# Kernel tuning notes

Hardware: AMD Instinct MI355X
Metric: run time of the kernel (lower is better)

Reference implementation:

```python
import jax, jax.numpy as jnp
import numpy as np

NEG_INF = float('-inf')

def setup_inputs() -> dict:
    key = jax.random.key(0)
    k1, k2 = jax.random.split(key)
    B, T, S, H, D = 2, 2048, 2048, 8, 64
    q = jax.random.normal(k1, (B, T, H, D), dtype=jnp.float32)
    kv = jax.random.normal(k2, (B, S, 2, H, D), dtype=jnp.float32)
    key_padding_mask = jnp.ones((B, S), dtype=bool)  # True = valid key
    return {"q": q, "kv": kv, "key_padding_mask": key_padding_mask, "causal": 1}


def reference(q, kv, key_padding_mask, causal):
    # q: (B,T,H,D), kv: (B,S,2,H,D)
    k = kv[:, :, 0]  # (B,S,H,D)
    v = kv[:, :, 1]  # (B,S,H,D)
    D = q.shape[-1]
    scale = D ** (-0.5)
    # scores: (B,H,T,S)
    scores = jnp.einsum('bthd,bshd->bhts', q, k) * scale
    # mask: True means "mask out" (matches torch masked_fill semantics)
    mask = ~key_padding_mask[:, None, None, :]  # (B,1,1,S)
    if causal:
        T, S = scores.shape[2], scores.shape[3]
        causal_mask = jnp.triu(jnp.ones((T, S), dtype=bool), k=1)  # (T,S)
        mask = mask | causal_mask[None, None, :, :]
    scores = jnp.where(mask, NEG_INF, scores)
    attn = jax.nn.softmax(scores, axis=-1)
    out = jnp.einsum('bhts,bshd->bthd', attn, v)  # (B,T,H,D)
    return out
```

## Files before the change

### kernel.cpp

```cpp
#include <hip/hip_runtime.h>
#include <hip/hip_bf16.h>
#include <math.h>

typedef __bf16 bf8_t __attribute__((ext_vector_type(8)));
typedef float  f4_t  __attribute__((ext_vector_type(4)));

constexpr int Bc = 2;
constexpr int Tc = 2048;
constexpr int Sc = 2048;
constexpr int Hc = 8;
constexpr int Dc = 64;
constexpr int BQ = 64;
constexpr int BK = 64;
constexpr int nQB = Tc / BQ;
constexpr int LDK = Dc + 8;
constexpr int LDV = BK + 2;
constexpr int SMAX = 8;
constexpr int GPH  = 144;

union BF8U { bf8_t v; unsigned int u[4]; };

__device__ inline unsigned int pkbf(float a, float b) {
    union { __bf16 h; unsigned short s; } x, y;
    x.h = (__bf16)a; y.h = (__bf16)b;
    return (unsigned int)x.s | ((unsigned int)y.s << 16);
}

__global__ __launch_bounds__(256, 4)
void fa_part(const float* __restrict__ q,
             const float* __restrict__ kv,
             const int* __restrict__ kpm,
             const int* __restrict__ causal_p,
             float* __restrict__ part_o,
             float* __restrict__ part_l)
{
    __shared__ __bf16 Ks[BK][LDK];
    __shared__ __bf16 Vt[Dc][LDV];

    const int tid  = threadIdx.x;
    const int wave = tid >> 6;
    const int lane = tid & 63;
    const int n16  = lane & 15;
    const int quad = lane >> 4;

    const int bid = blockIdx.x;
    const int h   = bid & 7;
    const int g   = bid >> 3;
    const int b   = g / GPH;
    const int idx = g - b * GPH;
    int a = (int)((sqrtf(1.0f + 2.0f * (float)idx) - 1.0f) * 0.5f);
    while (2 * (a + 1) * (a + 2) <= idx) ++a;
    while (2 * a * (a + 1) > idx) --a;
    const int rem = idx - 2 * a * (a + 1);
    const int S   = a + 1;
    const int r0  = rem / S;
    const int s   = rem - r0 * S;
    const int qt  = 4 * a + r0;
    const int q_base = qt * BQ;
    const int causal = causal_p[0];
    const int t_row  = q_base + wave * 16 + n16;

    {
        const int row = tid >> 2, dc = (tid & 3) * 16;
        const float* qr = q + ((size_t)(b * Tc + q_base + row) * Hc + h) * Dc + dc;
        float4 x[4];
        x[0] = *(const float4*)(qr + 0);
        x[1] = *(const float4*)(qr + 4);
        x[2] = *(const float4*)(qr + 8);
        x[3] = *(const float4*)(qr + 12);
        const float* xf = (const float*)x;
        const float sc = 0.125f;
        BF8U t0v, t1v;
        #pragma unroll
        for (int i = 0; i < 4; ++i) {
            t0v.u[i] = pkbf(xf[2 * i] * sc, xf[2 * i + 1] * sc);
            t1v.u[i] = pkbf(xf[8 + 2 * i] * sc, xf[9 + 2 * i] * sc);
        }
        *(bf8_t*)&Ks[row][dc]     = t0v.v;
        *(bf8_t*)&Ks[row][dc + 8] = t1v.v;
    }
    __syncthreads();
    bf8_t b_q[2];
    b_q[0] = *(const bf8_t*)&Ks[wave * 16 + n16][quad * 8];
    b_q[1] = *(const bf8_t*)&Ks[wave * 16 + n16][32 + quad * 8];

    f4_t o_acc[4];
    #pragma unroll
    for (int dt = 0; dt < 4; ++dt) o_acc[dt] = (f4_t){0.f, 0.f, 0.f, 0.f};
    float l_p = 0.f;

    const int kend = causal ? (q_base + BQ) : Sc;
    const int ntot = kend / BK;
    const int t0   = ntot * s / S;
    const int t1   = ntot * (s + 1) / S;

    const int krow = tid >> 2, kdc = (tid & 3) * 16;
    const int vkp  = tid >> 3, vdb = (tid & 7) * 8;
    const int KSTR = 2 * Hc * Dc;
    const float* kbase = kv + ((size_t)b * Sc * 2 * Hc + h) * Dc;
    const float* vbase = kbase + (size_t)Hc * Dc;

    float4 pk4[4], pv4[4];
    {
        const int kbG = t0 * BK;
        const float* kr = kbase + (size_t)(kbG + krow) * KSTR + kdc;
        pk4[0] = *(const float4*)(kr + 0);  pk4[1] = *(const float4*)(kr + 4);
        pk4[2] = *(const float4*)(kr + 8);  pk4[3] = *(const float4*)(kr + 12);
        const float* v0 = vbase + (size_t)(kbG + 2 * vkp) * KSTR + vdb;
        const float* v1 = v0 + KSTR;
        pv4[0] = *(const float4*)(v0 + 0);  pv4[1] = *(const float4*)(v0 + 4);
        pv4[2] = *(const float4*)(v1 + 0);  pv4[3] = *(const float4*)(v1 + 4);
    }

    for (int it = t0; it < t1; ++it) {
        const int kbG = it * BK;

        __syncthreads();

        {
            const float* kf = (const float*)pk4;
            BF8U w0, w1;
            #pragma unroll
            for (int i = 0; i < 4; ++i) {
                w0.u[i] = pkbf(kf[2 * i], kf[2 * i + 1]);
                w1.u[i] = pkbf(kf[8 + 2 * i], kf[9 + 2 * i]);
            }
            *(bf8_t*)&Ks[krow][kdc]     = w0.v;
            *(bf8_t*)&Ks[krow][kdc + 8] = w1.v;
            const float* vvf = (const float*)pv4;
            #pragma unroll
            for (int j = 0; j < 8; ++j) {
                *(unsigned int*)&Vt[vdb + j][2 * vkp] = pkbf(vvf[j], vvf[8 + j]);
            }
        }
        __syncthreads();

        if (it + 1 < t1) {
            const int nkb = kbG + BK;
            const float* kr = kbase + (size_t)(nkb + krow) * KSTR + kdc;
            pk4[0] = *(const float4*)(kr + 0);  pk4[1] = *(const float4*)(kr + 4);
            pk4[2] = *(const float4*)(kr + 8);  pk4[3] = *(const float4*)(kr + 12);
            const float* v0 = vbase + (size_t)(nkb + 2 * vkp) * KSTR + vdb;
            const float* v1 = v0 + KSTR;
            pv4[0] = *(const float4*)(v0 + 0);  pv4[1] = *(const float4*)(v0 + 4);
            pv4[2] = *(const float4*)(v1 + 0);  pv4[3] = *(const float4*)(v1 + 4);
        }

        f4_t sacc[4];
        #pragma unroll
        for (int u = 0; u < 4; ++u) {
            const bf8_t ak0 = *(const bf8_t*)&Ks[16 * u + n16][quad * 8];
            const bf8_t ak1 = *(const bf8_t*)&Ks[16 * u + n16][32 + quad * 8];
            f4_t acc = (f4_t){0.f, 0.f, 0.f, 0.f};
            acc = __builtin_amdgcn_mfma_f32_16x16x32_bf16(ak0, b_q[0], acc, 0, 0, 0);
            acc = __builtin_amdgcn_mfma_f32_16x16x32_bf16(ak1, b_q[1], acc, 0, 0, 0);
            sacc[u] = acc;
        }

        unsigned int pp[4][2];
        #pragma unroll
        for (int u = 0; u < 4; ++u) {
            const int4 mw = *(const int4*)&kpm[b * Sc + kbG + 16 * u + 4 * quad];
            float p[4];
            #pragma unroll
            for (int r = 0; r < 4; ++r) {
                const int key = kbG + 16 * u + 4 * quad + r;
                const bool valid = ((&mw.x)[r] != 0) && (!causal || key <= t_row);
                p[r] = valid ? __expf(sacc[u][r] - 8.0f) : 0.0f;
                l_p += p[r];
            }
            pp[u][0] = pkbf(p[0], p[1]);
            pp[u][1] = pkbf(p[2], p[3]);
        }

        const int sl0 = (2 * (quad & 1)) * 16 + n16;
        const int sl1 = sl0 + 16;
        int y[4][4];
        #pragma unroll
        for (int u = 0; u < 4; ++u) {
            y[u][0] = __shfl((int)pp[u][0], sl0, 64);
            y[u][1] = __shfl((int)pp[u][1], sl0, 64);
            y[u][2] = __shfl((int)pp[u][0], sl1, 64);
            y[u][3] = __shfl((int)pp[u][1], sl1, 64);
        }
        const bool hi = quad >= 2;
        BF8U bp0, bp1;
        #pragma unroll
        for (int i = 0; i < 4; ++i) {
            bp0.u[i] = (unsigned)(hi ? y[1][i] : y[0][i]);
            bp1.u[i] = (unsigned)(hi ? y[3][i] : y[2][i]);
        }

        #pragma unroll
        for (int dt = 0; dt < 4; ++dt) {
            const bf8_t av0 = *(const bf8_t*)&Vt[dt * 16 + n16][quad * 8];
            const bf8_t av1 = *(const bf8_t*)&Vt[dt * 16 + n16][32 + quad * 8];
            o_acc[dt] = __builtin_amdgcn_mfma_f32_16x16x32_bf16(av0, bp0.v, o_acc[dt], 0, 0, 0);
            o_acc[dt] = __builtin_amdgcn_mfma_f32_16x16x32_bf16(av1, bp1.v, o_acc[dt], 0, 0, 0);
        }
    }

    float l1 = l_p + __shfl_xor(l_p, 16, 64);
    const float l_tot = l1 + __shfl_xor(l1, 32, 64);

    const int qi  = (b * Hc + h) * nQB + qt;
    const int row = wave * 16 + n16;
    float* po = part_o + ((size_t)qi * SMAX + s) * (BQ * Dc);
    #pragma unroll
    for (int dt = 0; dt < 4; ++dt) {
        *(f4_t*)(po + row * Dc + dt * 16 + 4 * quad) = o_acc[dt];
    }
    if (quad == 0) {
        part_l[((size_t)qi * SMAX + s) * BQ + row] = l_tot;
    }
}

__global__ __launch_bounds__(256, 4)
void fa_reduce(const float* __restrict__ part_o,
               const float* __restrict__ part_l,
               float* __restrict__ out)
{
    const int gtid = blockIdx.x * 256 + threadIdx.x;
    const int e    = gtid & (BQ * Dc / 4 - 1);
    const int qi   = gtid >> 10;
    const int row  = e >> 4;
    const int d4   = e & 15;
    const int qt   = qi & (nQB - 1);
    const int S    = (qt >> 2) + 1;

    float4 acc = make_float4(0.f, 0.f, 0.f, 0.f);
    float  l   = 0.f;
    for (int s = 0; s < S; ++s) {
        const size_t pi = (size_t)qi * SMAX + s;
        const float4 v = *(const float4*)(part_o + pi * (BQ * Dc) + row * Dc + d4 * 4);
        acc.x += v.x; acc.y += v.y; acc.z += v.z; acc.w += v.w;
        l += part_l[pi * BQ + row];
    }
    const float inv = 1.0f / l;
    const int h = (qi / nQB) & (Hc - 1);
    const int b = qi / (nQB * Hc);
    const int t = qt * BQ + row;
    float4 o;
    o.x = acc.x * inv; o.y = acc.y * inv; o.z = acc.z * inv; o.w = acc.w * inv;
    *(float4*)(out + ((size_t)(b * Tc + t) * Hc + h) * Dc + d4 * 4) = o;
}

extern "C" void kernel_launch(void* const* d_in, const int* in_sizes, int n_in,
                              void* d_out, int out_size, void* d_ws, size_t ws_size,
                              hipStream_t stream) {
    const float* q   = (const float*)d_in[0];
    const float* kv  = (const float*)d_in[1];
    const int*   kpm = (const int*)d_in[2];
    const int*   cz  = (const int*)d_in[3];
    float*       out = (float*)d_out;

    const size_t nQT = (size_t)Bc * Hc * nQB;
    float* part_o = (float*)d_ws;
    float* part_l = part_o + nQT * SMAX * (BQ * Dc);

    const int grid1 = Bc * Hc * GPH;
    fa_part<<<grid1, 256, 0, stream>>>(q, kv, kpm, cz, part_o, part_l);
    const int grid2 = (int)(nQT * (BQ * Dc / 4) / 256);
    fa_reduce<<<grid2, 256, 0, stream>>>(part_o, part_l, out);
}
```

Baseline: 123.0 us.

## Route P through per-wave LDS, repad V tile, load Q directly to registers

Replaces the cross-lane shuffle transpose of the softmax probabilities with a per-wave LDS staging buffer (Ps), read back as MFMA B operands after an lgkmcnt wait. The V transpose now lives in a uint-packed tile padded to 33 words to reduce bank conflicts, and is read with scalar 32-bit LDS loads. Q fragments are loaded straight from global memory into registers, which drops the initial LDS round trip and one barrier. The mask loads are hoisted ahead of the QK MFMAs and the launch bound is raised to 5 blocks per CU. In exchange, extra LDS traffic and more LDS instructions per V read are added, and the larger shared footprint may limit the occupancy gain.

```diff
diff --git a/kernel.cpp b/kernel.cpp
--- a/kernel.cpp
+++ b/kernel.cpp
@@ -13,8 +13,9 @@
 constexpr int BQ = 64;
 constexpr int BK = 64;
 constexpr int nQB = Tc / BQ;
-constexpr int LDK = Dc + 8;
-constexpr int LDV = BK + 2;
+constexpr int LDK  = 72;
+constexpr int LDVP = 33;
+constexpr int LDP  = 72;
 constexpr int SMAX = 8;
 constexpr int GPH  = 144;
 
@@ -26,7 +27,7 @@
     return (unsigned int)x.s | ((unsigned int)y.s << 16);
 }
 
-__global__ __launch_bounds__(256, 4)
+__global__ __launch_bounds__(256, 5)
 void fa_part(const float* __restrict__ q,
              const float* __restrict__ kv,
              const int* __restrict__ kpm,
@@ -34,8 +35,9 @@
              float* __restrict__ part_o,
              float* __restrict__ part_l)
 {
-    __shared__ __bf16 Ks[BK][LDK];
-    __shared__ __bf16 Vt[Dc][LDV];
+    __shared__ __bf16        Ks[BK][LDK];
+    __shared__ unsigned int  VtP[Dc][LDVP];
+    __shared__ __bf16        Ps[4][16][LDP];
 
     const int tid  = threadIdx.x;
     const int wave = tid >> 6;
@@ -60,29 +62,22 @@
     const int causal = causal_p[0];
     const int t_row  = q_base + wave * 16 + n16;
 
+    bf8_t b_q[2];
     {
-        const int row = tid >> 2, dc = (tid & 3) * 16;
-        const float* qr = q + ((size_t)(b * Tc + q_base + row) * Hc + h) * Dc + dc;
-        float4 x[4];
-        x[0] = *(const float4*)(qr + 0);
-        x[1] = *(const float4*)(qr + 4);
-        x[2] = *(const float4*)(qr + 8);
-        x[3] = *(const float4*)(qr + 12);
-        const float* xf = (const float*)x;
+        const float* qrow = q + ((size_t)(b * Tc + t_row) * Hc + h) * Dc;
         const float sc = 0.125f;
-        BF8U t0v, t1v;
-        #pragma unroll
-        for (int i = 0; i < 4; ++i) {
-            t0v.u[i] = pkbf(xf[2 * i] * sc, xf[2 * i + 1] * sc);
-            t1v.u[i] = pkbf(xf[8 + 2 * i] * sc, xf[9 + 2 * i] * sc);
-        }
-        *(bf8_t*)&Ks[row][dc]     = t0v.v;
-        *(bf8_t*)&Ks[row][dc + 8] = t1v.v;
-    }
-    __syncthreads();
-    bf8_t b_q[2];
-    b_q[0] = *(const bf8_t*)&Ks[wave * 16 + n16][quad * 8];
-    b_q[1] = *(const bf8_t*)&Ks[wave * 16 + n16][32 + quad * 8];
+        #pragma unroll
+        for (int f = 0; f < 2; ++f) {
+            float4 x[2];
+            x[0] = *(const float4*)(qrow + f * 32 + quad * 8);
+            x[1] = *(const float4*)(qrow + f * 32 + quad * 8 + 4);
+            const float* xf = (const float*)x;
+            BF8U t;
+            #pragma unroll
+            for (int i = 0; i < 4; ++i) t.u[i] = pkbf(xf[2*i] * sc, xf[2*i+1] * sc);
+            b_q[f] = t.v;
+        }
+    }
 
     f4_t o_acc[4];
     #pragma unroll
@@ -99,9 +94,10 @@
     const int KSTR = 2 * Hc * Dc;
     const float* kbase = kv + ((size_t)b * Sc * 2 * Hc + h) * Dc;
     const float* vbase = kbase + (size_t)Hc * Dc;
+    const int* kpm_b = kpm + b * Sc;
 
     float4 pk4[4], pv4[4];
-    {
+    if (t0 < t1) {
         const int kbG = t0 * BK;
         const float* kr = kbase + (size_t)(kbG + krow) * KSTR + kdc;
         pk4[0] = *(const float4*)(kr + 0);  pk4[1] = *(const float4*)(kr + 4);
@@ -122,15 +118,15 @@
             BF8U w0, w1;
             #pragma unroll
             for (int i = 0; i < 4; ++i) {
-                w0.u[i] = pkbf(kf[2 * i], kf[2 * i + 1]);
-                w1.u[i] = pkbf(kf[8 + 2 * i], kf[9 + 2 * i]);
+                w0.u[i] = pkbf(kf[2*i],     kf[2*i+1]);
+                w1.u[i] = pkbf(kf[8+2*i],   kf[9+2*i]);
             }
             *(bf8_t*)&Ks[krow][kdc]     = w0.v;
             *(bf8_t*)&Ks[krow][kdc + 8] = w1.v;
             const float* vvf = (const float*)pv4;
             #pragma unroll
             for (int j = 0; j < 8; ++j) {
-                *(unsigned int*)&Vt[vdb + j][2 * vkp] = pkbf(vvf[j], vvf[8 + j]);
+                VtP[vdb + j][vkp] = pkbf(vvf[j], vvf[8 + j]);
             }
         }
         __syncthreads();
@@ -146,7 +142,11 @@
             pv4[2] = *(const float4*)(v1 + 0);  pv4[3] = *(const float4*)(v1 + 4);
         }
 
-        f4_t sacc[4];
+        int4 mw[4];
+        #pragma unroll
+        for (int u = 0; u < 4; ++u)
+            mw[u] = *(const int4*)&kpm_b[kbG + 16 * u + 4 * quad];
+
         #pragma unroll
         for (int u = 0; u < 4; ++u) {
             const bf8_t ak0 = *(const bf8_t*)&Ks[16 * u + n16][quad * 8];
@@ -154,49 +154,34 @@
             f4_t acc = (f4_t){0.f, 0.f, 0.f, 0.f};
             acc = __builtin_amdgcn_mfma_f32_16x16x32_bf16(ak0, b_q[0], acc, 0, 0, 0);
             acc = __builtin_amdgcn_mfma_f32_16x16x32_bf16(ak1, b_q[1], acc, 0, 0, 0);
-            sacc[u] = acc;
-        }
-
-        unsigned int pp[4][2];
-        #pragma unroll
-        for (int u = 0; u < 4; ++u) {
-            const int4 mw = *(const int4*)&kpm[b * Sc + kbG + 16 * u + 4 * quad];
             float p[4];
             #pragma unroll
             for (int r = 0; r < 4; ++r) {
                 const int key = kbG + 16 * u + 4 * quad + r;
-                const bool valid = ((&mw.x)[r] != 0) && (!causal || key <= t_row);
-                p[r] = valid ? __expf(sacc[u][r] - 8.0f) : 0.0f;
+                const bool valid = ((&mw[u].x)[r] != 0) && (!causal || key <= t_row);
+                p[r] = valid ? __expf(acc[r] - 8.0f) : 0.0f;
                 l_p += p[r];
             }
-            pp[u][0] = pkbf(p[0], p[1]);
-            pp[u][1] = pkbf(p[2], p[3]);
-        }
-
-        const int sl0 = (2 * (quad & 1)) * 16 + n16;
-        const int sl1 = sl0 + 16;
-        int y[4][4];
-        #pragma unroll
-        for (int u = 0; u < 4; ++u) {
-            y[u][0] = __shfl((int)pp[u][0], sl0, 64);
-            y[u][1] = __shfl((int)pp[u][1], sl0, 64);
-            y[u][2] = __shfl((int)pp[u][0], sl1, 64);
-            y[u][3] = __shfl((int)pp[u][1], sl1, 64);
-        }
-        const bool hi = quad >= 2;
-        BF8U bp0, bp1;
-        #pragma unroll
-        for (int i = 0; i < 4; ++i) {
-            bp0.u[i] = (unsigned)(hi ? y[1][i] : y[0][i]);
-            bp1.u[i] = (unsigned)(hi ? y[3][i] : y[2][i]);
-        }
+            *(uint2*)&Ps[wave][n16][16 * u + 4 * quad] =
+                make_uint2(pkbf(p[0], p[1]), pkbf(p[2], p[3]));
+        }
+
+        __asm__ volatile("s_waitcnt lgkmcnt(0)" ::: "memory");
+
+        const bf8_t bp0 = *(const bf8_t*)&Ps[wave][n16][quad * 8];
+        const bf8_t bp1 = *(const bf8_t*)&Ps[wave][n16][32 + quad * 8];
 
         #pragma unroll
         for (int dt = 0; dt < 4; ++dt) {
-            const bf8_t av0 = *(const bf8_t*)&Vt[dt * 16 + n16][quad * 8];
-            const bf8_t av1 = *(const bf8_t*)&Vt[dt * 16 + n16][32 + quad * 8];
-            o_acc[dt] = __builtin_amdgcn_mfma_f32_16x16x32_bf16(av0, bp0.v, o_acc[dt], 0, 0, 0);
-            o_acc[dt] = __builtin_amdgcn_mfma_f32_16x16x32_bf16(av1, bp1.v, o_acc[dt], 0, 0, 0);
+            const unsigned int* vrow = &VtP[dt * 16 + n16][0];
+            BF8U av0, av1;
+            #pragma unroll
+            for (int i = 0; i < 4; ++i) {
+                av0.u[i] = vrow[4 * quad + i];
+                av1.u[i] = vrow[16 + 4 * quad + i];
+            }
+            o_acc[dt] = __builtin_amdgcn_mfma_f32_16x16x32_bf16(av0.v, bp0, o_acc[dt], 0, 0, 0);
+            o_acc[dt] = __builtin_amdgcn_mfma_f32_16x16x32_bf16(av1.v, bp1, o_acc[dt], 0, 0, 0);
         }
     }
 
```

After: 123.4 us. About the same (+0.3%).
